# Optimization experiments

Hardware: AMD Instinct MI355X
Metric: run time of the kernel (lower is better)

Reference implementation:

```python
import jax, jax.numpy as jnp
import numpy as np

N = 100000      # nodes
E = 640000      # edges
VOCAB = 100     # Embedding(num_embeddings=100)
EMB = 10        # embed_dim
H = 128         # GCN hidden width


def gcn_conv(x, W, b, src, dst, n):
    """PyG GCNConv: linear (no bias) -> add self loops -> sym-normalized scatter-add -> +bias."""
    x = x @ W                                  # [n, out]
    loop = jnp.arange(n, dtype=src.dtype)
    src2 = jnp.concatenate([src, loop])        # [E+n]
    dst2 = jnp.concatenate([dst, loop])
    deg = jax.ops.segment_sum(jnp.ones_like(dst2, dtype=x.dtype), dst2, num_segments=n)
    dinv = jnp.where(deg > 0, jax.lax.rsqrt(deg), 0.0)
    norm = dinv[src2] * dinv[dst2]             # [E+n]
    out = jax.ops.segment_sum(x[src2] * norm[:, None], dst2, num_segments=n)
    return out + b


def setup_inputs() -> dict:
    key = jax.random.key(0)
    ks = jax.random.split(key, 9)
    x = jax.random.randint(ks[0], (N, 1), 0, VOCAB, dtype=jnp.int32)
    edge_index = jax.random.randint(ks[1], (2, E), 0, N, dtype=jnp.int32)
    batch = jnp.zeros((N,), dtype=jnp.int32)
    emb = jax.random.normal(ks[2], (VOCAB, EMB), dtype=jnp.float32)
    W1 = jax.random.normal(ks[3], (EMB, H), dtype=jnp.float32) * 0.1
    b1 = jnp.zeros((H,), dtype=jnp.float32)
    W2 = jax.random.normal(ks[4], (H, H), dtype=jnp.float32) * 0.1
    b2 = jnp.zeros((H,), dtype=jnp.float32)
    W3 = jax.random.normal(ks[5], (H, 1), dtype=jnp.float32) * 0.1
    b3 = jnp.zeros((1,), dtype=jnp.float32)
    return {"x": x, "edge_index": edge_index, "batch": batch,
            "emb": emb, "W1": W1, "b1": b1, "W2": W2, "b2": b2, "W3": W3, "b3": b3}


def reference(x, edge_index, batch, emb, W1, b1, W2, b2, W3, b3):
    # eval mode: dropout(p=0.5) is identity
    h = emb[x[:, 0]]                           # [N, EMB] embedding lookup + squeeze
    src, dst = edge_index[0], edge_index[1]
    n = h.shape[0]
    h = jax.nn.relu(gcn_conv(h, W1, b1, src, dst, n))   # [N, 128]
    h = jax.nn.relu(gcn_conv(h, W2, b2, src, dst, n))   # [N, 128]
    out = jax.nn.sigmoid((h @ W3 + b3).reshape(-1))      # [N]
    return out
```

## Files before the change

### kernel.cpp

```cpp
#include <hip/hip_runtime.h>
#include <math.h>

#define HDIM 128
#define EMBD 10
#define CAP  64
#define BSTRIDE 136

typedef __attribute__((ext_vector_type(8))) short short8;
typedef __attribute__((ext_vector_type(8))) unsigned short ushort8;
typedef __attribute__((ext_vector_type(4))) float float4a;

__device__ inline ushort bf16_rne(float f) {
    unsigned u = __float_as_uint(f);
    unsigned r = (u + 0x7fffu + ((u >> 16) & 1u)) >> 16;
    return (ushort)r;
}
__device__ inline float bf16_to_f(ushort u) {
    return __uint_as_float(((unsigned)u) << 16);
}

__global__ void k_table(const float* __restrict__ emb, const float* __restrict__ W1,
                        float* __restrict__ T, int vocab) {
    int t = blockIdx.x * blockDim.x + threadIdx.x;
    if (t >= vocab * HDIM) return;
    int c = t >> 7, f = t & 127;
    float s = 0.f;
#pragma unroll
    for (int k = 0; k < EMBD; ++k) s += emb[c * EMBD + k] * W1[k * HDIM + f];
    T[t] = s;
}

__global__ void k_fill(const int* __restrict__ src, const int* __restrict__ dst,
                       int* __restrict__ cnt, int* __restrict__ slot, int E) {
    int e = blockIdx.x * blockDim.x + threadIdx.x;
    if (e >= E) return;
    int d = dst[e];
    int p = atomicAdd(&cnt[d], 1);
    if (p < CAP) slot[(size_t)d * CAP + p] = src[e];
}

__global__ void k_gather1(const int* __restrict__ slot, const int* __restrict__ cnt,
                          const int* __restrict__ x, const float* __restrict__ T,
                          const float* __restrict__ b1, ushort* __restrict__ A, int N) {
    int tid = blockIdx.x * 256 + threadIdx.x;
    int v = tid >> 4, q = tid & 15;
    if (v >= N) return;
    int deg = cnt[v];
    int m = min(deg, CAP);
    float acc[8] = {0.f, 0.f, 0.f, 0.f, 0.f, 0.f, 0.f, 0.f};
    for (int base = 0; base < m; base += 16) {
        int j = base + q;
        int cls = 0; float w = 0.f;
        if (j < m) {
            int s = slot[(size_t)v * CAP + j];
            cls = x[s];
            w = rsqrtf((float)cnt[s] + 1.0f);
        }
        int lim = min(m - base, 16);
#pragma unroll 2
        for (int t = 0; t < lim; ++t) {
            int c   = __shfl(cls, t, 16);
            float ww = __shfl(w, t, 16);
            const float* tr = T + c * HDIM + q * 8;
            float4 t0 = *(const float4*)tr;
            float4 t1 = *(const float4*)(tr + 4);
            acc[0] += ww * t0.x; acc[1] += ww * t0.y;
            acc[2] += ww * t0.z; acc[3] += ww * t0.w;
            acc[4] += ww * t1.x; acc[5] += ww * t1.y;
            acc[6] += ww * t1.z; acc[7] += ww * t1.w;
        }
    }
    float dv = rsqrtf((float)deg + 1.0f);
    float dd = dv * dv;
    const float* tr = T + x[v] * HDIM + q * 8;
    float4 t0 = *(const float4*)tr;
    float4 t1 = *(const float4*)(tr + 4);
    float4 bb0 = *(const float4*)(b1 + q * 8);
    float4 bb1 = *(const float4*)(b1 + q * 8 + 4);
    float ts[8] = {t0.x, t0.y, t0.z, t0.w, t1.x, t1.y, t1.z, t1.w};
    float bb[8] = {bb0.x, bb0.y, bb0.z, bb0.w, bb1.x, bb1.y, bb1.z, bb1.w};
    ushort8 o;
#pragma unroll
    for (int k = 0; k < 8; ++k)
        o[k] = bf16_rne(fmaxf(dv * acc[k] + dd * ts[k] + bb[k], 0.f));
    *(ushort8*)(A + (size_t)v * HDIM + q * 8) = o;
}

__global__ __launch_bounds__(256) void k_gemm2(const ushort* __restrict__ Abf,
                                               const float* __restrict__ W2,
                                               ushort* __restrict__ Y, int N) {
    __shared__ ushort Bt[HDIM * BSTRIDE];
    for (int i = threadIdx.x; i < HDIM * HDIM; i += 256) {
        int k = i >> 7, n = i & 127;
        Bt[n * BSTRIDE + k] = bf16_rne(W2[i]);
    }
    __syncthreads();

    int lane = threadIdx.x & 63;
    int wid  = threadIdx.x >> 6;
    int half = wid & 1;
    int rw   = (blockIdx.x * 4 + wid) >> 1;
    int nrw  = gridDim.x * 2;
    int l15  = lane & 15, quad = lane >> 4;

    short8 bfrag[4][4];
#pragma unroll
    for (int nt = 0; nt < 4; ++nt)
#pragma unroll
        for (int kt = 0; kt < 4; ++kt) {
            int n = half * 64 + nt * 16 + l15;
            int k = kt * 32 + quad * 8;
            bfrag[nt][kt] = *(const short8*)&Bt[n * BSTRIDE + k];
        }

    int nchunks = (N + 63) >> 6;
    for (int ch = rw; ch < nchunks; ch += nrw) {
        int m0 = ch * 64;
        short8 afrag[4][4];
#pragma unroll
        for (int mt = 0; mt < 4; ++mt)
#pragma unroll
            for (int kt = 0; kt < 4; ++kt) {
                int m = m0 + mt * 16 + l15;
                if (m >= N) m = N - 1;
                int k = kt * 32 + quad * 8;
                afrag[mt][kt] = *(const short8*)&Abf[(size_t)m * HDIM + k];
            }
#pragma unroll
        for (int nt = 0; nt < 4; ++nt) {
            float4a acc[4] = {{0.f,0.f,0.f,0.f},{0.f,0.f,0.f,0.f},
                              {0.f,0.f,0.f,0.f},{0.f,0.f,0.f,0.f}};
#pragma unroll
            for (int mt = 0; mt < 4; ++mt)
#pragma unroll
                for (int kt = 0; kt < 4; ++kt)
                    acc[mt] = __builtin_amdgcn_mfma_f32_16x16x32_bf16(
                        afrag[mt][kt], bfrag[nt][kt], acc[mt], 0, 0, 0);
            int col = half * 64 + nt * 16 + l15;
#pragma unroll
            for (int mt = 0; mt < 4; ++mt) {
                int row0 = m0 + mt * 16 + quad * 4;
#pragma unroll
                for (int r = 0; r < 4; ++r) {
                    int row = row0 + r;
                    if (row < N) Y[(size_t)row * HDIM + col] = bf16_rne(acc[mt][r]);
                }
            }
        }
    }
}

__global__ void k_gather2(const int* __restrict__ slot, const int* __restrict__ cnt,
                          const ushort* __restrict__ Y, const float* __restrict__ b2,
                          const float* __restrict__ W3, const float* __restrict__ b3,
                          float* __restrict__ out, int N) {
    int tid = blockIdx.x * 256 + threadIdx.x;
    int v = tid >> 4, q = tid & 15;
    if (v >= N) return;
    int deg = cnt[v];
    int m = min(deg, CAP);
    float acc[8] = {0.f, 0.f, 0.f, 0.f, 0.f, 0.f, 0.f, 0.f};
    for (int base = 0; base < m; base += 16) {
        int j = base + q;
        int sj = 0; float wj = 0.f;
        if (j < m) {
            sj = slot[(size_t)v * CAP + j];
            wj = rsqrtf((float)cnt[sj] + 1.0f);
        }
        int lim = min(m - base, 16);
        int t = 0;
        for (; t + 4 <= lim; t += 4) {
            int s0 = __shfl(sj, t, 16),     s1 = __shfl(sj, t + 1, 16);
            int s2 = __shfl(sj, t + 2, 16), s3 = __shfl(sj, t + 3, 16);
            float w0 = __shfl(wj, t, 16),     w1 = __shfl(wj, t + 1, 16);
            float w2 = __shfl(wj, t + 2, 16), w3v = __shfl(wj, t + 3, 16);
            ushort8 y0 = *(const ushort8*)(Y + (size_t)s0 * HDIM + q * 8);
            ushort8 y1 = *(const ushort8*)(Y + (size_t)s1 * HDIM + q * 8);
            ushort8 y2 = *(const ushort8*)(Y + (size_t)s2 * HDIM + q * 8);
            ushort8 y3 = *(const ushort8*)(Y + (size_t)s3 * HDIM + q * 8);
#pragma unroll
            for (int k = 0; k < 8; ++k) acc[k] += w0 * bf16_to_f(y0[k]);
#pragma unroll
            for (int k = 0; k < 8; ++k) acc[k] += w1 * bf16_to_f(y1[k]);
#pragma unroll
            for (int k = 0; k < 8; ++k) acc[k] += w2 * bf16_to_f(y2[k]);
#pragma unroll
            for (int k = 0; k < 8; ++k) acc[k] += w3v * bf16_to_f(y3[k]);
        }
        for (; t < lim; ++t) {
            int s0 = __shfl(sj, t, 16);
            float w0 = __shfl(wj, t, 16);
            ushort8 y0 = *(const ushort8*)(Y + (size_t)s0 * HDIM + q * 8);
#pragma unroll
            for (int k = 0; k < 8; ++k) acc[k] += w0 * bf16_to_f(y0[k]);
        }
    }
    float dv = rsqrtf((float)deg + 1.0f);
    float dd = dv * dv;
    ushort8 ys = *(const ushort8*)(Y + (size_t)v * HDIM + q * 8);
    float4 bb0 = *(const float4*)(b2 + q * 8);
    float4 bb1 = *(const float4*)(b2 + q * 8 + 4);
    float4 w30 = *(const float4*)(W3 + q * 8);
    float4 w31 = *(const float4*)(W3 + q * 8 + 4);
    float bb[8] = {bb0.x, bb0.y, bb0.z, bb0.w, bb1.x, bb1.y, bb1.z, bb1.w};
    float w3a[8] = {w30.x, w30.y, w30.z, w30.w, w31.x, w31.y, w31.z, w31.w};
    float p = 0.f;
#pragma unroll
    for (int k = 0; k < 8; ++k)
        p += fmaxf(dv * acc[k] + dd * bf16_to_f(ys[k]) + bb[k], 0.f) * w3a[k];
#pragma unroll
    for (int off = 8; off; off >>= 1) p += __shfl_xor(p, off, 16);
    if (q == 0) out[v] = 1.f / (1.f + expf(-(p + b3[0])));
}

extern "C" void kernel_launch(void* const* d_in, const int* in_sizes, int n_in,
                              void* d_out, int out_size, void* d_ws, size_t ws_size,
                              hipStream_t stream) {
    const int*   x    = (const int*)d_in[0];
    const int*   ei   = (const int*)d_in[1];
    const float* emb  = (const float*)d_in[3];
    const float* W1   = (const float*)d_in[4];
    const float* b1   = (const float*)d_in[5];
    const float* W2   = (const float*)d_in[6];
    const float* b2   = (const float*)d_in[7];
    const float* W3   = (const float*)d_in[8];
    const float* b3   = (const float*)d_in[9];
    float*       out  = (float*)d_out;

    int N = in_sizes[0];
    int E = in_sizes[1] / 2;
    int vocab = in_sizes[3] / EMBD;
    const int* src = ei;
    const int* dst = ei + E;

    char* w = (char*)d_ws;
    float*  T    = (float*)w;   w += (size_t)vocab * HDIM * 4;
    ushort* A    = (ushort*)w;  w += (size_t)N * HDIM * 2;
    ushort* Y    = (ushort*)w;  w += (size_t)N * HDIM * 2;
    int*    cnt  = (int*)w;     w += (size_t)N * 4;
    int*    slot = (int*)w;     w += (size_t)N * CAP * 4;

    hipMemsetAsync(cnt, 0, (size_t)N * sizeof(int), stream);
    k_table<<<(vocab * HDIM + 255) / 256, 256, 0, stream>>>(emb, W1, T, vocab);
    k_fill<<<(E + 255) / 256, 256, 0, stream>>>(src, dst, cnt, slot, E);

    int gblocks = (int)(((long long)N * 16 + 255) / 256);
    k_gather1<<<gblocks, 256, 0, stream>>>(slot, cnt, x, T, b1, A, N);
    k_gemm2<<<512, 256, 0, stream>>>(A, W2, Y, N);
    k_gather2<<<gblocks, 256, 0, stream>>>(slot, cnt, Y, b2, W3, b3, out, N);
}
```

Before: 187.0 us.

## Fuse layer-2 aggregation, GEMM and output head into one kernel

Reorders layer 2 so that neighbour aggregation runs first on the layer-1 activations. The aggregated 16-row tiles are staged in LDS and multiplied by a pre-transposed bf16 W2 with MFMA, and bias, ReLU, the W3 dot product and the sigmoid are applied in the same kernel. This removes the separate GEMM pass and the round trip of the intermediate Y matrix through global memory. It also folds the count memset, the embedding table and the W2 transpose into one prep kernel. In exchange, each wave reads W2 fragments from global or cache, and the aggregated values are rounded to bf16 before the GEMM.

```diff
diff --git a/kernel.cpp b/kernel.cpp
--- a/kernel.cpp
+++ b/kernel.cpp
@@ -4,7 +4,7 @@
 #define HDIM 128
 #define EMBD 10
 #define CAP  64
-#define BSTRIDE 136
+#define ZSTRIDE 136
 
 typedef __attribute__((ext_vector_type(8))) short short8;
 typedef __attribute__((ext_vector_type(8))) unsigned short ushort8;
@@ -19,15 +19,23 @@
     return __uint_as_float(((unsigned)u) << 16);
 }
 
-__global__ void k_table(const float* __restrict__ emb, const float* __restrict__ W1,
-                        float* __restrict__ T, int vocab) {
-    int t = blockIdx.x * blockDim.x + threadIdx.x;
-    if (t >= vocab * HDIM) return;
-    int c = t >> 7, f = t & 127;
-    float s = 0.f;
-#pragma unroll
-    for (int k = 0; k < EMBD; ++k) s += emb[c * EMBD + k] * W1[k * HDIM + f];
-    T[t] = s;
+__global__ void k_prep(const float* __restrict__ emb, const float* __restrict__ W1,
+                       const float* __restrict__ W2, float* __restrict__ T,
+                       ushort* __restrict__ W2t, int* __restrict__ cnt,
+                       int N, int vocab) {
+    int t = blockIdx.x * 256 + threadIdx.x;
+    if (t < N) cnt[t] = 0;
+    if (t < vocab * HDIM) {
+        int c = t >> 7, f = t & 127;
+        float s = 0.f;
+#pragma unroll
+        for (int k = 0; k < EMBD; ++k) s += emb[c * EMBD + k] * W1[k * HDIM + f];
+        T[t] = s;
+    }
+    if (t < HDIM * HDIM) {
+        int n = t >> 7, k = t & 127;
+        W2t[t] = bf16_rne(W2[k * HDIM + n]);
+    }
 }
 
 __global__ void k_fill(const int* __restrict__ src, const int* __restrict__ dst,
@@ -59,7 +67,7 @@
         int lim = min(m - base, 16);
 #pragma unroll 2
         for (int t = 0; t < lim; ++t) {
-            int c   = __shfl(cls, t, 16);
+            int c    = __shfl(cls, t, 16);
             float ww = __shfl(w, t, 16);
             const float* tr = T + c * HDIM + q * 8;
             float4 t0 = *(const float4*)tr;
@@ -86,131 +94,117 @@
     *(ushort8*)(A + (size_t)v * HDIM + q * 8) = o;
 }
 
-__global__ __launch_bounds__(256) void k_gemm2(const ushort* __restrict__ Abf,
-                                               const float* __restrict__ W2,
-                                               ushort* __restrict__ Y, int N) {
-    __shared__ ushort Bt[HDIM * BSTRIDE];
-    for (int i = threadIdx.x; i < HDIM * HDIM; i += 256) {
-        int k = i >> 7, n = i & 127;
-        Bt[n * BSTRIDE + k] = bf16_rne(W2[i]);
-    }
-    __syncthreads();
-
+__global__ __launch_bounds__(256) void k_conv2(const int* __restrict__ slot,
+                                               const int* __restrict__ cnt,
+                                               const ushort* __restrict__ A,
+                                               const ushort* __restrict__ W2t,
+                                               const float* __restrict__ b2,
+                                               const float* __restrict__ W3,
+                                               const float* __restrict__ b3,
+                                               float* __restrict__ out, int N) {
+    __shared__ ushort Z[4][16 * ZSTRIDE];
     int lane = threadIdx.x & 63;
     int wid  = threadIdx.x >> 6;
-    int half = wid & 1;
-    int rw   = (blockIdx.x * 4 + wid) >> 1;
-    int nrw  = gridDim.x * 2;
-    int l15  = lane & 15, quad = lane >> 4;
-
-    short8 bfrag[4][4];
-#pragma unroll
-    for (int nt = 0; nt < 4; ++nt)
-#pragma unroll
-        for (int kt = 0; kt < 4; ++kt) {
-            int n = half * 64 + nt * 16 + l15;
-            int k = kt * 32 + quad * 8;
-            bfrag[nt][kt] = *(const short8*)&Bt[n * BSTRIDE + k];
-        }
-
-    int nchunks = (N + 63) >> 6;
-    for (int ch = rw; ch < nchunks; ch += nrw) {
-        int m0 = ch * 64;
-        short8 afrag[4][4];
-#pragma unroll
-        for (int mt = 0; mt < 4; ++mt)
-#pragma unroll
-            for (int kt = 0; kt < 4; ++kt) {
-                int m = m0 + mt * 16 + l15;
-                if (m >= N) m = N - 1;
-                int k = kt * 32 + quad * 8;
-                afrag[mt][kt] = *(const short8*)&Abf[(size_t)m * HDIM + k];
-            }
-#pragma unroll
-        for (int nt = 0; nt < 4; ++nt) {
-            float4a acc[4] = {{0.f,0.f,0.f,0.f},{0.f,0.f,0.f,0.f},
-                              {0.f,0.f,0.f,0.f},{0.f,0.f,0.f,0.f}};
-#pragma unroll
-            for (int mt = 0; mt < 4; ++mt)
-#pragma unroll
-                for (int kt = 0; kt < 4; ++kt)
-                    acc[mt] = __builtin_amdgcn_mfma_f32_16x16x32_bf16(
-                        afrag[mt][kt], bfrag[nt][kt], acc[mt], 0, 0, 0);
-            int col = half * 64 + nt * 16 + l15;
-#pragma unroll
-            for (int mt = 0; mt < 4; ++mt) {
-                int row0 = m0 + mt * 16 + quad * 4;
-#pragma unroll
-                for (int r = 0; r < 4; ++r) {
-                    int row = row0 + r;
-                    if (row < N) Y[(size_t)row * HDIM + col] = bf16_rne(acc[mt][r]);
+    int q16  = lane & 15;
+    int g4   = lane >> 4;
+    int tile = blockIdx.x * 4 + wid;
+    int v0   = tile * 16;
+
+    if (v0 < N) {
+        for (int r = 0; r < 4; ++r) {
+            int vr = v0 + r * 4 + g4;
+            int v = min(vr, N - 1);
+            int deg = cnt[v];
+            int m = min(deg, CAP);
+            float acc[8] = {0.f, 0.f, 0.f, 0.f, 0.f, 0.f, 0.f, 0.f};
+            for (int base = 0; base < m; base += 16) {
+                int j = base + q16;
+                int sj = 0; float wj = 0.f;
+                if (j < m) {
+                    sj = slot[(size_t)v * CAP + j];
+                    wj = rsqrtf((float)cnt[sj] + 1.0f);
+                }
+                int lim = min(m - base, 16);
+                int t = 0;
+                for (; t + 4 <= lim; t += 4) {
+                    int s0 = __shfl(sj, t, 16),     s1 = __shfl(sj, t + 1, 16);
+                    int s2 = __shfl(sj, t + 2, 16), s3 = __shfl(sj, t + 3, 16);
+                    float w0 = __shfl(wj, t, 16),     w1 = __shfl(wj, t + 1, 16);
+                    float w2 = __shfl(wj, t + 2, 16), w3v = __shfl(wj, t + 3, 16);
+                    ushort8 y0 = *(const ushort8*)(A + (size_t)s0 * HDIM + q16 * 8);
+                    ushort8 y1 = *(const ushort8*)(A + (size_t)s1 * HDIM + q16 * 8);
+                    ushort8 y2 = *(const ushort8*)(A + (size_t)s2 * HDIM + q16 * 8);
+                    ushort8 y3 = *(const ushort8*)(A + (size_t)s3 * HDIM + q16 * 8);
+#pragma unroll
+                    for (int k = 0; k < 8; ++k) acc[k] += w0 * bf16_to_f(y0[k]);
+#pragma unroll
+                    for (int k = 0; k < 8; ++k) acc[k] += w1 * bf16_to_f(y1[k]);
+#pragma unroll
+                    for (int k = 0; k < 8; ++k) acc[k] += w2 * bf16_to_f(y2[k]);
+#pragma unroll
+                    for (int k = 0; k < 8; ++k) acc[k] += w3v * bf16_to_f(y3[k]);
+                }
+                for (; t < lim; ++t) {
+                    int s0 = __shfl(sj, t, 16);
+                    float w0 = __shfl(wj, t, 16);
+                    ushort8 y0 = *(const ushort8*)(A + (size_t)s0 * HDIM + q16 * 8);
+#pragma unroll
+                    for (int k = 0; k < 8; ++k) acc[k] += w0 * bf16_to_f(y0[k]);
                 }
             }
-        }
-    }
-}
-
-__global__ void k_gather2(const int* __restrict__ slot, const int* __restrict__ cnt,
-                          const ushort* __restrict__ Y, const float* __restrict__ b2,
-                          const float* __restrict__ W3, const float* __restrict__ b3,
-                          float* __restrict__ out, int N) {
-    int tid = blockIdx.x * 256 + threadIdx.x;
-    int v = tid >> 4, q = tid & 15;
-    if (v >= N) return;
-    int deg = cnt[v];
-    int m = min(deg, CAP);
-    float acc[8] = {0.f, 0.f, 0.f, 0.f, 0.f, 0.f, 0.f, 0.f};
-    for (int base = 0; base < m; base += 16) {
-        int j = base + q;
-        int sj = 0; float wj = 0.f;
-        if (j < m) {
-            sj = slot[(size_t)v * CAP + j];
-            wj = rsqrtf((float)cnt[sj] + 1.0f);
-        }
-        int lim = min(m - base, 16);
-        int t = 0;
-        for (; t + 4 <= lim; t += 4) {
-            int s0 = __shfl(sj, t, 16),     s1 = __shfl(sj, t + 1, 16);
-            int s2 = __shfl(sj, t + 2, 16), s3 = __shfl(sj, t + 3, 16);
-            float w0 = __shfl(wj, t, 16),     w1 = __shfl(wj, t + 1, 16);
-            float w2 = __shfl(wj, t + 2, 16), w3v = __shfl(wj, t + 3, 16);
-            ushort8 y0 = *(const ushort8*)(Y + (size_t)s0 * HDIM + q * 8);
-            ushort8 y1 = *(const ushort8*)(Y + (size_t)s1 * HDIM + q * 8);
-            ushort8 y2 = *(const ushort8*)(Y + (size_t)s2 * HDIM + q * 8);
-            ushort8 y3 = *(const ushort8*)(Y + (size_t)s3 * HDIM + q * 8);
-#pragma unroll
-            for (int k = 0; k < 8; ++k) acc[k] += w0 * bf16_to_f(y0[k]);
-#pragma unroll
-            for (int k = 0; k < 8; ++k) acc[k] += w1 * bf16_to_f(y1[k]);
-#pragma unroll
-            for (int k = 0; k < 8; ++k) acc[k] += w2 * bf16_to_f(y2[k]);
-#pragma unroll
-            for (int k = 0; k < 8; ++k) acc[k] += w3v * bf16_to_f(y3[k]);
-        }
-        for (; t < lim; ++t) {
-            int s0 = __shfl(sj, t, 16);
-            float w0 = __shfl(wj, t, 16);
-            ushort8 y0 = *(const ushort8*)(Y + (size_t)s0 * HDIM + q * 8);
-#pragma unroll
-            for (int k = 0; k < 8; ++k) acc[k] += w0 * bf16_to_f(y0[k]);
-        }
-    }
-    float dv = rsqrtf((float)deg + 1.0f);
-    float dd = dv * dv;
-    ushort8 ys = *(const ushort8*)(Y + (size_t)v * HDIM + q * 8);
-    float4 bb0 = *(const float4*)(b2 + q * 8);
-    float4 bb1 = *(const float4*)(b2 + q * 8 + 4);
-    float4 w30 = *(const float4*)(W3 + q * 8);
-    float4 w31 = *(const float4*)(W3 + q * 8 + 4);
-    float bb[8] = {bb0.x, bb0.y, bb0.z, bb0.w, bb1.x, bb1.y, bb1.z, bb1.w};
-    float w3a[8] = {w30.x, w30.y, w30.z, w30.w, w31.x, w31.y, w31.z, w31.w};
-    float p = 0.f;
-#pragma unroll
-    for (int k = 0; k < 8; ++k)
-        p += fmaxf(dv * acc[k] + dd * bf16_to_f(ys[k]) + bb[k], 0.f) * w3a[k];
-#pragma unroll
-    for (int off = 8; off; off >>= 1) p += __shfl_xor(p, off, 16);
-    if (q == 0) out[v] = 1.f / (1.f + expf(-(p + b3[0])));
+            float dv = rsqrtf((float)deg + 1.0f);
+            float dd = dv * dv;
+            ushort8 ys = *(const ushort8*)(A + (size_t)v * HDIM + q16 * 8);
+            ushort8 z;
+#pragma unroll
+            for (int k = 0; k < 8; ++k)
+                z[k] = bf16_rne(dv * acc[k] + dd * bf16_to_f(ys[k]));
+            *(ushort8*)&Z[wid][(r * 4 + g4) * ZSTRIDE + q16 * 8] = z;
+        }
+    }
+    __syncthreads();
+    if (v0 >= N) return;
+
+    short8 af[4];
+#pragma unroll
+    for (int kt = 0; kt < 4; ++kt)
+        af[kt] = *(const short8*)&Z[wid][q16 * ZSTRIDE + kt * 32 + g4 * 8];
+
+    float4a accD[8];
+#pragma unroll
+    for (int nt = 0; nt < 8; ++nt) accD[nt] = (float4a){0.f, 0.f, 0.f, 0.f};
+#pragma unroll
+    for (int nt = 0; nt < 8; ++nt) {
+        const ushort* bp = W2t + (size_t)(nt * 16 + q16) * HDIM + g4 * 8;
+#pragma unroll
+        for (int kt = 0; kt < 4; ++kt) {
+            short8 bf = *(const short8*)(bp + kt * 32);
+            accD[nt] = __builtin_amdgcn_mfma_f32_16x16x32_bf16(af[kt], bf, accD[nt], 0, 0, 0);
+        }
+    }
+
+    float p[4] = {0.f, 0.f, 0.f, 0.f};
+#pragma unroll
+    for (int nt = 0; nt < 8; ++nt) {
+        int col = nt * 16 + q16;
+        float bc = b2[col], wc = W3[col];
+#pragma unroll
+        for (int r = 0; r < 4; ++r)
+            p[r] += fmaxf(accD[nt][r] + bc, 0.f) * wc;
+    }
+#pragma unroll
+    for (int off = 1; off < 16; off <<= 1) {
+#pragma unroll
+        for (int r = 0; r < 4; ++r) p[r] += __shfl_xor(p[r], off, 16);
+    }
+    if (q16 == 0) {
+        float b3v = b3[0];
+#pragma unroll
+        for (int r = 0; r < 4; ++r) {
+            int row = v0 + g4 * 4 + r;
+            if (row < N) out[row] = 1.f / (1.f + expf(-(p[r] + b3v)));
+        }
+    }
 }
 
 extern "C" void kernel_launch(void* const* d_in, const int* in_sizes, int n_in,
@@ -236,16 +230,19 @@
     char* w = (char*)d_ws;
     float*  T    = (float*)w;   w += (size_t)vocab * HDIM * 4;
     ushort* A    = (ushort*)w;  w += (size_t)N * HDIM * 2;
-    ushort* Y    = (ushort*)w;  w += (size_t)N * HDIM * 2;
+    ushort* W2t  = (ushort*)w;  w += (size_t)HDIM * HDIM * 2;
     int*    cnt  = (int*)w;     w += (size_t)N * 4;
     int*    slot = (int*)w;     w += (size_t)N * CAP * 4;
 
-    hipMemsetAsync(cnt, 0, (size_t)N * sizeof(int), stream);
-    k_table<<<(vocab * HDIM + 255) / 256, 256, 0, stream>>>(emb, W1, T, vocab);
+    int prep_elems = N;
+    if (vocab * HDIM > prep_elems) prep_elems = vocab * HDIM;
+    if (HDIM * HDIM > prep_elems) prep_elems = HDIM * HDIM;
+    k_prep<<<(prep_elems + 255) / 256, 256, 0, stream>>>(emb, W1, W2, T, W2t, cnt, N, vocab);
     k_fill<<<(E + 255) / 256, 256, 0, stream>>>(src, dst, cnt, slot, E);
 
     int gblocks = (int)(((long long)N * 16 + 255) / 256);
     k_gather1<<<gblocks, 256, 0, stream>>>(slot, cnt, x, T, b1, A, N);
-    k_gemm2<<<512, 256, 0, stream>>>(A, W2, Y, N);
-    k_gather2<<<gblocks, 256, 0, stream>>>(slot, cnt, Y, b2, W3, b3, out, N);
-}
+
+    int ntiles = (N + 15) / 16;
+    k_conv2<<<(ntiles + 3) / 4, 256, 0, stream>>>(slot, cnt, A, W2t, b2, W3, b3, out, N);
+}
```

New measurement: 199.3 us. 1.07x slower.
